# Kernel optimization log

Hardware: AMD Instinct MI355X
Metric: run time of the kernel (lower is better)

Reference implementation:

```python
import jax, jax.numpy as jnp
import numpy as np

B, S, N_CLASS = 16, 2048, 8
T0, T1 = 0.0, 100.0
EPS = 1e-8


def setup_inputs() -> dict:
    key = jax.random.key(0)
    k1, k2, k3, k4, k5 = jax.random.split(key, 5)
    # event times sorted along the sequence dim (Hawkes history is causal)
    ts = jnp.sort(jax.random.uniform(k1, (B, S), minval=0.0, maxval=T1, dtype=jnp.float32), axis=1)
    ms = jax.random.randint(k2, (B, S), 0, N_CLASS, dtype=jnp.int32)
    mu = jax.random.uniform(k3, (N_CLASS,), minval=0.05, maxval=0.2, dtype=jnp.float32)
    alphas = jax.random.uniform(k4, (N_CLASS, N_CLASS), minval=0.01, maxval=0.1, dtype=jnp.float32)
    beta = jax.random.uniform(k5, (N_CLASS,), minval=0.5, maxval=2.0, dtype=jnp.float32)
    return {"ts": ts, "ms": ms, "mu": mu, "alphas": alphas, "beta": beta}


def reference(ts, ms, mu, alphas, beta):
    # ts: [B,S] float times; ms: [B,S] int event types
    valid = ts > 0                                          # [B,S]
    # causal pair mask j < i, combined with event validity of both endpoints
    tri = jnp.tril(jnp.ones((S, S), dtype=bool), k=-1)      # [S,S]
    pair_valid = tri[None, :, :] & valid[:, :, None] & valid[:, None, :]
    # time differences t_i - t_j, zeroed where masked (avoids exp overflow)
    tds = jnp.where(pair_valid, ts[:, :, None] - ts[:, None, :], 0.0)
    a_ij = alphas[ms[:, :, None], ms[:, None, :]]           # [B,S,S] alpha[m_i, m_j]
    b_j = beta[ms][:, None, :]                              # [B,1,S] beta[m_j]
    K = a_ij * b_j * jnp.exp(-b_j * tds) * pair_valid       # [B,S,S]
    lams = K.sum(-1) + mu[ms]                               # [B,S]
    sumlog = (jnp.log(lams + EPS) * valid).sum()
    baserate = mu.sum() * (T1 - T0)
    # compensator integral: sum_i alpha[:,m_i].sum() * (1 - exp(-beta[m_i]*(T1 - t_i)))
    temp_int = 1.0 - jnp.exp(-beta[ms] * (T1 - ts))         # [B,S]
    alpha_int = alphas[:, ms].sum(0)                        # [B,S]
    integ = (alpha_int * temp_int * valid).sum()
    return sumlog - baserate - integ
```

## Files before the change

### kernel.cpp

```cpp
#include <hip/hip_runtime.h>
#include <math.h>

#define BB 16
#define SS 2048
#define NC 8
#define TILE 128
#define NT (SS/TILE)
#define LOG2E 1.4426950408889634f
#define LN2   0.6931471805599453f
#define T1V 100.0f
#define EPSV 1e-8f

__device__ __forceinline__ float fexp2(float x) {
#if __has_builtin(__builtin_amdgcn_exp2f)
    return __builtin_amdgcn_exp2f(x);
#else
    return exp2f(x);
#endif
}
__device__ __forceinline__ float flog2(float x) {
#if __has_builtin(__builtin_amdgcn_logf)
    return __builtin_amdgcn_logf(x);
#else
    return log2f(x);
#endif
}

__global__ __launch_bounds__(TILE) void hawkes_tilesum(
    const float* __restrict__ ts, const int* __restrict__ ms,
    const float* __restrict__ beta, float* __restrict__ E)
{
    int b = blockIdx.x / NT;
    int T = blockIdx.x % NT;
    int tid = threadIdx.x;
    int jg = b*SS + T*TILE + tid;

    float tj = ts[jg];
    int   mj = ms[jg];
    float tref = ts[b*SS + T*TILE + TILE-1];
    float p  = beta[mj] * LOG2E;
    float e  = (tj > 0.0f) ? fexp2(p * (tj - tref)) : 0.0f;

    int lane = tid & 63, wave = tid >> 6;
    __shared__ float shw[2*NC];
    #pragma unroll
    for (int c = 0; c < NC; ++c) {
        float v = (mj == c) ? e : 0.0f;
        for (int off = 32; off; off >>= 1) v += __shfl_xor(v, off, 64);
        if (lane == 0) shw[wave*NC + c] = v;
    }
    __syncthreads();
    if (tid < NC) E[(b*NT + T)*NC + tid] = shw[tid] + shw[NC + tid];
}

__global__ __launch_bounds__(TILE) void hawkes_main(
    const float* __restrict__ ts, const int* __restrict__ ms,
    const float* __restrict__ mu, const float* __restrict__ alphas,
    const float* __restrict__ beta, const float* __restrict__ E,
    float* __restrict__ out)
{
    int b = blockIdx.x / NT;
    int T = blockIdx.x % NT;
    int tid = threadIdx.x;

    __shared__ float sh_ab[NC*NC];
    __shared__ float sh_acol[NC];
    __shared__ float sh_pc[NC];
    __shared__ float sh_g[NC];
    __shared__ float sh_pu[TILE];
    __shared__ float sh_p[TILE];
    __shared__ int   sh_m[TILE];

    if (tid < NC*NC) {
        int col = tid & (NC-1);
        sh_ab[tid] = alphas[tid] * beta[col];
    }
    if (tid < NC) {
        float s = 0.0f;
        #pragma unroll
        for (int r = 0; r < NC; ++r) s += alphas[r*NC + tid];
        sh_acol[tid] = s;
        sh_pc[tid] = beta[tid] * LOG2E;
    }

    int ig = b*SS + T*TILE + tid;
    float ti = ts[ig];
    int   mi = ms[ig];
    float pi = beta[mi] * LOG2E;
    sh_p[tid]  = pi;
    sh_pu[tid] = (ti > 0.0f) ? pi * ti : -1e30f;
    sh_m[tid]  = mi;

    float anchor = (T > 0) ? ts[b*SS + T*TILE - 1] : 0.0f;
    if (tid < NC) {
        float g = 0.0f;
        if (T > 0) {
            float pc = beta[tid] * LOG2E;
            for (int Tp = 0; Tp < T; ++Tp) {
                float tr = ts[b*SS + Tp*TILE + TILE-1];
                g += fexp2(pc * (tr - anchor)) * E[(b*NT + Tp)*NC + tid];
            }
        }
        sh_g[tid] = g;
    }
    __syncthreads();

    const float* abrow = &sh_ab[mi*NC];
    float acc = 0.0f;

    if (T > 0) {
        #pragma unroll
        for (int c = 0; c < NC; ++c) {
            float dec = fexp2(sh_pc[c] * (anchor - ti));
            acc = fmaf(abrow[c] * sh_g[c], dec, acc);
        }
    }

    int wave = tid >> 6, lane = tid & 63;
    int jfull = wave * 64;
    for (int j = 0; j < jfull; ++j) {
        float arg = fmaf(-sh_p[j], ti, sh_pu[j]);
        acc = fmaf(abrow[sh_m[j]], fexp2(arg), acc);
    }
    #pragma unroll 4
    for (int jj = 0; jj < 64; ++jj) {
        int j = jfull + jj;
        float arg = fmaf(-sh_p[j], ti, sh_pu[j]);
        float v = (jj < lane) ? abrow[sh_m[j]] * fexp2(arg) : 0.0f;
        acc += v;
    }

    float contrib = 0.0f;
    if (ti > 0.0f) {
        float lam = acc + mu[mi];
        contrib = flog2(lam + EPSV) * LN2;
        float tint = 1.0f - fexp2(-pi * (T1V - ti));
        contrib -= sh_acol[mi] * tint;
    }

    for (int off = 32; off; off >>= 1) contrib += __shfl_xor(contrib, off, 64);
    __shared__ float shred[2];
    if (lane == 0) shred[wave] = contrib;
    __syncthreads();
    if (tid == 0) atomicAdd(out, shred[0] + shred[1]);

    if (blockIdx.x == 0 && tid == 0) {
        float msum = 0.0f;
        #pragma unroll
        for (int c = 0; c < NC; ++c) msum += mu[c];
        atomicAdd(out, -msum * (T1V - 0.0f));
    }
}

extern "C" void kernel_launch(void* const* d_in, const int* in_sizes, int n_in,
                              void* d_out, int out_size, void* d_ws, size_t ws_size,
                              hipStream_t stream) {
    const float* ts     = (const float*)d_in[0];
    const int*   ms     = (const int*)d_in[1];
    const float* mu     = (const float*)d_in[2];
    const float* alphas = (const float*)d_in[3];
    const float* beta   = (const float*)d_in[4];
    float* out = (float*)d_out;
    float* E   = (float*)d_ws;

    hipMemsetAsync(out, 0, sizeof(float), stream);
    hawkes_tilesum<<<BB*NT, TILE, 0, stream>>>(ts, ms, beta, E);
    hawkes_main<<<BB*NT, TILE, 0, stream>>>(ts, ms, mu, alphas, beta, E, out);
}
```

Measured before the change: 75.59 us.

## Fuse tile-sum and main kernels into one cooperative launch with in-block prefix recompute

Drops the separate tile-summary kernel. Each block now directly recomputes the decayed per-class sums of all earlier events in its batch row, relative to its own anchor. The memset and atomic accumulation are replaced by per-block partials that block 0 reduces after a cooperative grid sync. This removes two launches and the memset, at the cost of redundant prefix work that grows with tile index and the overhead of a grid-wide barrier.

```diff
diff --git a/kernel.cpp b/kernel.cpp
--- a/kernel.cpp
+++ b/kernel.cpp
@@ -1,11 +1,15 @@
 #include <hip/hip_runtime.h>
+#include <hip/hip_cooperative_groups.h>
 #include <math.h>
+
+namespace cg = cooperative_groups;
 
 #define BB 16
 #define SS 2048
 #define NC 8
 #define TILE 128
 #define NT (SS/TILE)
+#define NBLK (BB*NT)
 #define LOG2E 1.4426950408889634f
 #define LN2   0.6931471805599453f
 #define T1V 100.0f
@@ -26,42 +30,16 @@
 #endif
 }
 
-__global__ __launch_bounds__(TILE) void hawkes_tilesum(
-    const float* __restrict__ ts, const int* __restrict__ ms,
-    const float* __restrict__ beta, float* __restrict__ E)
-{
-    int b = blockIdx.x / NT;
-    int T = blockIdx.x % NT;
-    int tid = threadIdx.x;
-    int jg = b*SS + T*TILE + tid;
-
-    float tj = ts[jg];
-    int   mj = ms[jg];
-    float tref = ts[b*SS + T*TILE + TILE-1];
-    float p  = beta[mj] * LOG2E;
-    float e  = (tj > 0.0f) ? fexp2(p * (tj - tref)) : 0.0f;
-
-    int lane = tid & 63, wave = tid >> 6;
-    __shared__ float shw[2*NC];
-    #pragma unroll
-    for (int c = 0; c < NC; ++c) {
-        float v = (mj == c) ? e : 0.0f;
-        for (int off = 32; off; off >>= 1) v += __shfl_xor(v, off, 64);
-        if (lane == 0) shw[wave*NC + c] = v;
-    }
-    __syncthreads();
-    if (tid < NC) E[(b*NT + T)*NC + tid] = shw[tid] + shw[NC + tid];
-}
-
-__global__ __launch_bounds__(TILE) void hawkes_main(
+__global__ __launch_bounds__(TILE) void hawkes_fused(
     const float* __restrict__ ts, const int* __restrict__ ms,
     const float* __restrict__ mu, const float* __restrict__ alphas,
-    const float* __restrict__ beta, const float* __restrict__ E,
+    const float* __restrict__ beta, float* __restrict__ part,
     float* __restrict__ out)
 {
-    int b = blockIdx.x / NT;
-    int T = blockIdx.x % NT;
-    int tid = threadIdx.x;
+    const int b    = blockIdx.x / NT;
+    const int T    = blockIdx.x % NT;
+    const int tid  = threadIdx.x;
+    const int lane = tid & 63, wave = tid >> 6;
 
     __shared__ float sh_ab[NC*NC];
     __shared__ float sh_acol[NC];
@@ -70,10 +48,14 @@
     __shared__ float sh_pu[TILE];
     __shared__ float sh_p[TILE];
     __shared__ int   sh_m[TILE];
+    __shared__ float shred[2*NC];
+
+    const int   ig = b*SS + T*TILE + tid;
+    const float ti = ts[ig];
+    const int   mi = ms[ig];
 
     if (tid < NC*NC) {
-        int col = tid & (NC-1);
-        sh_ab[tid] = alphas[tid] * beta[col];
+        sh_ab[tid] = alphas[tid] * beta[tid & (NC-1)];
     }
     if (tid < NC) {
         float s = 0.0f;
@@ -83,26 +65,33 @@
         sh_pc[tid] = beta[tid] * LOG2E;
     }
 
-    int ig = b*SS + T*TILE + tid;
-    float ti = ts[ig];
-    int   mi = ms[ig];
-    float pi = beta[mi] * LOG2E;
+    const float pi = beta[mi] * LOG2E;
     sh_p[tid]  = pi;
     sh_pu[tid] = (ti > 0.0f) ? pi * ti : -1e30f;
     sh_m[tid]  = mi;
 
-    float anchor = (T > 0) ? ts[b*SS + T*TILE - 1] : 0.0f;
-    if (tid < NC) {
-        float g = 0.0f;
-        if (T > 0) {
-            float pc = beta[tid] * LOG2E;
-            for (int Tp = 0; Tp < T; ++Tp) {
-                float tr = ts[b*SS + Tp*TILE + TILE-1];
-                g += fexp2(pc * (tr - anchor)) * E[(b*NT + Tp)*NC + tid];
-            }
-        }
-        sh_g[tid] = g;
+    const float anchor = (T > 0) ? ts[b*SS + T*TILE - 1] : 0.0f;
+    __syncthreads();
+
+    float gcl[NC];
+    #pragma unroll
+    for (int c = 0; c < NC; ++c) gcl[c] = 0.0f;
+    for (int base = 0; base < T*TILE; base += TILE) {
+        const int   jg = b*SS + base + tid;
+        const float tj = ts[jg];
+        const int   mj = ms[jg];
+        const float e  = (tj > 0.0f) ? fexp2(sh_pc[mj] * (tj - anchor)) : 0.0f;
+        #pragma unroll
+        for (int c = 0; c < NC; ++c) gcl[c] += (mj == c) ? e : 0.0f;
     }
+    #pragma unroll
+    for (int c = 0; c < NC; ++c) {
+        float v = gcl[c];
+        for (int off = 32; off; off >>= 1) v += __shfl_xor(v, off, 64);
+        if (lane == 0) shred[wave*NC + c] = v;
+    }
+    __syncthreads();
+    if (tid < NC) sh_g[tid] = shred[tid] + shred[NC + tid];
     __syncthreads();
 
     const float* abrow = &sh_ab[mi*NC];
@@ -111,44 +100,49 @@
     if (T > 0) {
         #pragma unroll
         for (int c = 0; c < NC; ++c) {
-            float dec = fexp2(sh_pc[c] * (anchor - ti));
+            const float dec = fexp2(sh_pc[c] * (anchor - ti));
             acc = fmaf(abrow[c] * sh_g[c], dec, acc);
         }
     }
 
-    int wave = tid >> 6, lane = tid & 63;
-    int jfull = wave * 64;
+    const int jfull = wave * 64;
     for (int j = 0; j < jfull; ++j) {
-        float arg = fmaf(-sh_p[j], ti, sh_pu[j]);
+        const float arg = fmaf(-sh_p[j], ti, sh_pu[j]);
         acc = fmaf(abrow[sh_m[j]], fexp2(arg), acc);
     }
     #pragma unroll 4
     for (int jj = 0; jj < 64; ++jj) {
-        int j = jfull + jj;
-        float arg = fmaf(-sh_p[j], ti, sh_pu[j]);
-        float v = (jj < lane) ? abrow[sh_m[j]] * fexp2(arg) : 0.0f;
+        const int j = jfull + jj;
+        const float arg = fmaf(-sh_p[j], ti, sh_pu[j]);
+        const float v = (jj < lane) ? abrow[sh_m[j]] * fexp2(arg) : 0.0f;
         acc += v;
     }
 
     float contrib = 0.0f;
     if (ti > 0.0f) {
-        float lam = acc + mu[mi];
+        const float lam = acc + mu[mi];
         contrib = flog2(lam + EPSV) * LN2;
-        float tint = 1.0f - fexp2(-pi * (T1V - ti));
+        const float tint = 1.0f - fexp2(-pi * (T1V - ti));
         contrib -= sh_acol[mi] * tint;
     }
-
     for (int off = 32; off; off >>= 1) contrib += __shfl_xor(contrib, off, 64);
-    __shared__ float shred[2];
     if (lane == 0) shred[wave] = contrib;
     __syncthreads();
-    if (tid == 0) atomicAdd(out, shred[0] + shred[1]);
+    if (tid == 0) part[blockIdx.x] = shred[0] + shred[1];
 
-    if (blockIdx.x == 0 && tid == 0) {
-        float msum = 0.0f;
-        #pragma unroll
-        for (int c = 0; c < NC; ++c) msum += mu[c];
-        atomicAdd(out, -msum * (T1V - 0.0f));
+    cg::this_grid().sync();
+
+    if (blockIdx.x == 0) {
+        float v = part[tid] + part[tid + TILE];
+        for (int off = 32; off; off >>= 1) v += __shfl_xor(v, off, 64);
+        if (lane == 0) shred[wave] = v;
+        __syncthreads();
+        if (tid == 0) {
+            float msum = 0.0f;
+            #pragma unroll
+            for (int c = 0; c < NC; ++c) msum += mu[c];
+            out[0] = shred[0] + shred[1] - msum * (T1V - 0.0f);
+        }
     }
 }
 
@@ -160,10 +154,11 @@
     const float* mu     = (const float*)d_in[2];
     const float* alphas = (const float*)d_in[3];
     const float* beta   = (const float*)d_in[4];
-    float* out = (float*)d_out;
-    float* E   = (float*)d_ws;
+    float* out  = (float*)d_out;
+    float* part = (float*)d_ws;
 
-    hipMemsetAsync(out, 0, sizeof(float), stream);
-    hawkes_tilesum<<<BB*NT, TILE, 0, stream>>>(ts, ms, beta, E);
-    hawkes_main<<<BB*NT, TILE, 0, stream>>>(ts, ms, mu, alphas, beta, E, out);
+    void* args[] = { (void*)&ts, (void*)&ms, (void*)&mu, (void*)&alphas,
+                     (void*)&beta, (void*)&part, (void*)&out };
+    hipLaunchCooperativeKernel((void*)hawkes_fused, dim3(NBLK), dim3(TILE),
+                               args, 0, stream);
 }
```

Measured after the change: 112.3 us. +48.6%, slower.
